# Kernel optimization log

Hardware: AMD Instinct MI355X
Metric: run time of the kernel (lower is better)

The kernel has to match this reference:

```python
import jax, jax.numpy as jnp
import numpy as np

B, H, W = 64, 16, 16
DIMS = [2048, 1024, 512, 256, 128, 1]


def _target_fc(x, w, b):
    # x: [B, in, H, W]; w: [B, out, in, 1, 1]; b: [B, out]
    # Equivalent to grouped 1x1 conv2d with groups=B (per-sample FC over channels).
    y = jnp.einsum('boi,bihw->bohw', w[:, :, :, 0, 0], x)
    return y + b[:, :, None, None]


def setup_inputs() -> dict:
    key = jax.random.key(0)
    ks = jax.random.split(key, 11)
    inp = {'x': jax.random.normal(ks[0], (B, DIMS[0], H, W), dtype=jnp.float32)}
    for i in range(5):
        din, dout = DIMS[i], DIMS[i + 1]
        scale = 1.0 / np.sqrt(din)
        inp[f'w{i+1}'] = jax.random.normal(ks[1 + 2 * i], (B, dout, din, 1, 1), dtype=jnp.float32) * scale
        inp[f'b{i+1}'] = jax.random.normal(ks[2 + 2 * i], (B, dout), dtype=jnp.float32) * scale
    return inp


def reference(x, w1, b1, w2, b2, w3, b3, w4, b4, w5, b5):
    q = jax.nn.sigmoid(_target_fc(x, w1, b1))
    q = jax.nn.sigmoid(_target_fc(q, w2, b2))
    q = jax.nn.sigmoid(_target_fc(q, w3, b3))
    q = jax.nn.sigmoid(_target_fc(q, w4, b4))
    q = _target_fc(q, w5, b5)
    return jnp.squeeze(q)  # [B, H, W]
```

## Files before the change

kernel.cpp:

```cpp
#include <hip/hip_runtime.h>
#include <hip/hip_bf16.h>
#include <cstdint>

#define DEVINL __device__ __forceinline__

typedef __attribute__((ext_vector_type(8))) short bf16x8;
typedef __attribute__((ext_vector_type(4))) float f32x4;

DEVINL unsigned short f2bf(float f) {
    union { float f; unsigned u; } v; v.f = f;
    unsigned r = v.u + 0x7fffu + ((v.u >> 16) & 1u);
    return (unsigned short)(r >> 16);
}
DEVINL float bf2f(unsigned short h) {
    union { unsigned u; float f; } v; v.u = ((unsigned)h) << 16;
    return v.f;
}

constexpr int BM = 64, BN = 256, BK = 32;
constexpr int PA  = 40;
constexpr int NSP = 256;

__global__ __launch_bounds__(256)
void xpose(const float* __restrict__ x, unsigned short* __restrict__ xT)
{
    __shared__ float sh[64][65];
    const int b   = blockIdx.y;
    const int kt  = blockIdx.x & 31;
    const int ntb = blockIdx.x >> 5;
    const int k0 = kt * 64, n0 = ntb * 64;

    const int r = threadIdx.x >> 4;
    const int c = (threadIdx.x & 15) * 4;

    const float* xb = x + ((size_t)b * 2048 + k0) * 256 + n0;
#pragma unroll
    for (int i = 0; i < 4; ++i) {
        float4 v = *(const float4*)(xb + (size_t)(r + 16 * i) * 256 + c);
        sh[r + 16 * i][c + 0] = v.x;
        sh[r + 16 * i][c + 1] = v.y;
        sh[r + 16 * i][c + 2] = v.z;
        sh[r + 16 * i][c + 3] = v.w;
    }
    __syncthreads();
#pragma unroll
    for (int i = 0; i < 4; ++i) {
        const int rr = r + 16 * i;
        ushort4 o;
        o.x = f2bf(sh[c + 0][rr]);
        o.y = f2bf(sh[c + 1][rr]);
        o.z = f2bf(sh[c + 2][rr]);
        o.w = f2bf(sh[c + 3][rr]);
        *(ushort4*)(xT + ((size_t)b * NSP + n0 + rr) * 2048 + k0 + c) = o;
    }
}

__global__ __launch_bounds__(256, 4)
void fc_gemm(const float* __restrict__ Wt, const float* __restrict__ bias,
             const unsigned short* __restrict__ X, unsigned short* __restrict__ Yt,
             int M, int K)
{
    const int b  = blockIdx.x;
    const int m0 = blockIdx.y * BM;

    __shared__ __align__(128) unsigned short pool[64 * PA + 2 * 256 * 32];
    unsigned short* sA = pool;
    unsigned short* sB = pool + 64 * PA;

    const int tid  = threadIdx.x;
    const int lane = tid & 63;
    const int wid  = tid >> 6;
    const int wn   = wid * 64;
    const int fr   = lane & 15;
    const int fo   = (lane >> 4) * 8;

    const int am = tid >> 2, ac = (tid & 3) * 8;
    const float* Wb = Wt + (size_t)b * M * K + (size_t)m0 * K + (size_t)am * K + ac;

    const int grow = wid * 64 + (lane >> 2);
    const int gchk = ((lane & 3) ^ ((lane >> 3) & 3)) * 8;
    const unsigned short* Xb = X + (size_t)b * NSP * K;

    const int bslot = ((lane >> 4) ^ ((fr >> 1) & 3)) * 8;

    const int NT = K / BK;

    float4 aS[2];

#define LOADA(k0) { aS[0] = *(const float4*)(Wb + (k0)); \
                    aS[1] = *(const float4*)(Wb + (k0) + 4); }
#define STOREA()  { ushort4 p0, p1; \
        p0.x = f2bf(aS[0].x); p0.y = f2bf(aS[0].y); p0.z = f2bf(aS[0].z); p0.w = f2bf(aS[0].w); \
        p1.x = f2bf(aS[1].x); p1.y = f2bf(aS[1].y); p1.z = f2bf(aS[1].z); p1.w = f2bf(aS[1].w); \
        *(ushort4*)&sA[am * PA + ac]     = p0; \
        *(ushort4*)&sA[am * PA + ac + 4] = p1; }
#define GLOADB(k0, bufofs) { \
    _Pragma("unroll") for (int i = 0; i < 4; ++i) { \
        const unsigned short* src_ = Xb + (size_t)(grow + i * 16) * K + (k0) + gchk; \
        const unsigned short* dst_ = sB + (bufofs) + (wid * 64 + i * 16) * 32; \
        __builtin_amdgcn_global_load_lds( \
            (const __attribute__((address_space(1))) void*)src_, \
            (__attribute__((address_space(3))) void*)dst_, 16, 0, 0); } }

    f32x4 acc[4][4] = {};

    LOADA(0)
    GLOADB(0, 0)
    STOREA()
    __syncthreads();

#pragma unroll 1
    for (int t = 0; t < NT; ++t) {
        const int pr = (t & 1) * (256 * 32);
        const int pw = ((t + 1) & 1) * (256 * 32);
        if (t + 1 < NT) { LOADA((t + 1) * BK) GLOADB((t + 1) * BK, pw) }

        bf16x8 af[4], bf[4];
#pragma unroll
        for (int i = 0; i < 4; ++i)
            af[i] = *(const bf16x8*)&sA[(i * 16 + fr) * PA + fo];
#pragma unroll
        for (int i = 0; i < 4; ++i)
            bf[i] = *(const bf16x8*)&sB[pr + (wn + i * 16 + fr) * 32 + bslot];

        asm volatile("s_waitcnt lgkmcnt(0)" ::: "memory");
        __builtin_amdgcn_s_barrier();

        if (t + 1 < NT) STOREA()

#pragma unroll
        for (int mi = 0; mi < 4; ++mi)
#pragma unroll
            for (int ni = 0; ni < 4; ++ni)
                acc[mi][ni] = __builtin_amdgcn_mfma_f32_16x16x32_bf16(af[mi], bf[ni], acc[mi][ni], 0, 0, 0);

        __syncthreads();
    }
#undef LOADA
#undef STOREA
#undef GLOADB

    const int hi4 = (lane >> 4) * 4;
#pragma unroll 1
    for (int ph = 0; ph < 2; ++ph) {
        if ((wn >> 7) == ph) {
#pragma unroll
            for (int mi = 0; mi < 4; ++mi) {
#pragma unroll
                for (int ni = 0; ni < 4; ++ni) {
                    const int r  = (wn & 127) + ni * 16 + fr;
                    const int mb = mi * 16 + hi4;
                    f32x4 v = acc[mi][ni];
                    ushort4 o;
#pragma unroll
                    for (int q = 0; q < 4; ++q) {
                        float yv = v[q] + bias[(size_t)b * M + m0 + mb + q];
                        yv = 1.0f / (1.0f + __expf(-yv));
                        ((unsigned short*)&o)[q] = f2bf(yv);
                    }
                    *(ushort4*)&pool[r * 72 + mb] = o;
                }
            }
        }
        __syncthreads();
        const int r = tid >> 3;
        const int c = (tid & 7) * 8;
#pragma unroll
        for (int it = 0; it < 4; ++it) {
            const int rr = r + it * 32;
            uint4 v = *(const uint4*)&pool[rr * 72 + c];
            *(uint4*)&Yt[((size_t)b * NSP + ph * 128 + rr) * M + m0 + c] = v;
        }
        __syncthreads();
    }
}

__global__ void fc_final(const unsigned short* __restrict__ A4,
                         const float* __restrict__ W5,
                         const float* __restrict__ B5,
                         float* __restrict__ out)
{
    const int b = blockIdx.x;
    const int t = threadIdx.x;
    const unsigned short* row = A4 + ((size_t)b * NSP + t) * 128;
    const float* w = W5 + (size_t)b * 128;
    float acc = B5[b];
#pragma unroll
    for (int k = 0; k < 128; k += 8) {
        uint4 v = *(const uint4*)(row + k);
        acc += bf2f((unsigned short)(v.x & 0xffff)) * w[k+0];
        acc += bf2f((unsigned short)(v.x >> 16))    * w[k+1];
        acc += bf2f((unsigned short)(v.y & 0xffff)) * w[k+2];
        acc += bf2f((unsigned short)(v.y >> 16))    * w[k+3];
        acc += bf2f((unsigned short)(v.z & 0xffff)) * w[k+4];
        acc += bf2f((unsigned short)(v.z >> 16))    * w[k+5];
        acc += bf2f((unsigned short)(v.w & 0xffff)) * w[k+6];
        acc += bf2f((unsigned short)(v.w >> 16))    * w[k+7];
    }
    out[b * NSP + t] = acc;
}

extern "C" void kernel_launch(void* const* d_in, const int* in_sizes, int n_in,
                              void* d_out, int out_size, void* d_ws, size_t ws_size,
                              hipStream_t stream)
{
    const float* x  = (const float*)d_in[0];
    const float* w1 = (const float*)d_in[1];
    const float* b1 = (const float*)d_in[2];
    const float* w2 = (const float*)d_in[3];
    const float* b2 = (const float*)d_in[4];
    const float* w3 = (const float*)d_in[5];
    const float* b3 = (const float*)d_in[6];
    const float* w4 = (const float*)d_in[7];
    const float* b4 = (const float*)d_in[8];
    const float* w5 = (const float*)d_in[9];
    const float* b5 = (const float*)d_in[10];

    unsigned short* ws0 = (unsigned short*)d_ws;

    const size_t XT = (size_t)64 * 256 * 2048;
    unsigned short* xT   = ws0;
    unsigned short* act1 = ws0 + XT;
    unsigned short* act2 = ws0;
    unsigned short* act3 = ws0 + (size_t)64 * 256 * 512;
    unsigned short* act4 = ws0 + (size_t)64 * 256 * (512 + 256);

    xpose<<<dim3(128, 64), dim3(256), 0, stream>>>(x, xT);
    fc_gemm<<<dim3(64, 16), dim3(256), 0, stream>>>(w1, b1, xT,   act1, 1024, 2048);
    fc_gemm<<<dim3(64,  8), dim3(256), 0, stream>>>(w2, b2, act1, act2,  512, 1024);
    fc_gemm<<<dim3(64,  4), dim3(256), 0, stream>>>(w3, b3, act2, act3,  256,  512);
    fc_gemm<<<dim3(64,  2), dim3(256), 0, stream>>>(w4, b4, act3, act4,  128,  256);
    fc_final<<<dim3(64), dim3(256), 0, stream>>>(act4, w5, b5, (float*)d_out);
}
```

Before: 372.8 us.

## Fuse transpose and all FC layers into one persistent kernel with per-sample barriers

Replaces six launches (transpose, four GEMMs, final dot) with a single kernel of 512 blocks, eight blocks per sample, synchronized by a per-sample global atomic barrier between layers. This removes launch gaps and lets later small layers follow immediately. In exchange, later layers leave most blocks idle (only 4 or 2 of 8 work), the barrier relies on all 512 blocks being co-resident, and layer 1 now runs in 512 blocks rather than 1024. A memset is added to reset the barrier counters.

```diff
diff --git a/kernel.cpp b/kernel.cpp
--- a/kernel.cpp
+++ b/kernel.cpp
@@ -21,53 +21,43 @@
 constexpr int PA  = 40;
 constexpr int NSP = 256;
 
-__global__ __launch_bounds__(256)
-void xpose(const float* __restrict__ x, unsigned short* __restrict__ xT)
-{
-    __shared__ float sh[64][65];
-    const int b   = blockIdx.y;
-    const int kt  = blockIdx.x & 31;
-    const int ntb = blockIdx.x >> 5;
-    const int k0 = kt * 64, n0 = ntb * 64;
-
-    const int r = threadIdx.x >> 4;
-    const int c = (threadIdx.x & 15) * 4;
-
-    const float* xb = x + ((size_t)b * 2048 + k0) * 256 + n0;
-#pragma unroll
-    for (int i = 0; i < 4; ++i) {
-        float4 v = *(const float4*)(xb + (size_t)(r + 16 * i) * 256 + c);
-        sh[r + 16 * i][c + 0] = v.x;
-        sh[r + 16 * i][c + 1] = v.y;
-        sh[r + 16 * i][c + 2] = v.z;
-        sh[r + 16 * i][c + 3] = v.w;
-    }
+constexpr size_t ARENA  = 1048576;
+constexpr size_t XT_OFF = 0;
+constexpr size_t A1_OFF = 524288;
+constexpr size_t A2_OFF = 786432;
+constexpr size_t A3_OFF = 917504;
+constexpr size_t A4_OFF = 983040;
+constexpr size_t BAR_BYTE_OFF = (size_t)64 * ARENA * 2;
+
+DEVINL void gbar(unsigned* cnt, unsigned* gen)
+{
     __syncthreads();
-#pragma unroll
-    for (int i = 0; i < 4; ++i) {
-        const int rr = r + 16 * i;
-        ushort4 o;
-        o.x = f2bf(sh[c + 0][rr]);
-        o.y = f2bf(sh[c + 1][rr]);
-        o.z = f2bf(sh[c + 2][rr]);
-        o.w = f2bf(sh[c + 3][rr]);
-        *(ushort4*)(xT + ((size_t)b * NSP + n0 + rr) * 2048 + k0 + c) = o;
-    }
-}
-
-__global__ __launch_bounds__(256, 4)
-void fc_gemm(const float* __restrict__ Wt, const float* __restrict__ bias,
-             const unsigned short* __restrict__ X, unsigned short* __restrict__ Yt,
-             int M, int K)
-{
-    const int b  = blockIdx.x;
-    const int m0 = blockIdx.y * BM;
-
-    __shared__ __align__(128) unsigned short pool[64 * PA + 2 * 256 * 32];
+    if (threadIdx.x == 0) {
+        unsigned g = __hip_atomic_load(gen, __ATOMIC_RELAXED, __HIP_MEMORY_SCOPE_AGENT);
+        __threadfence();
+        unsigned v = __hip_atomic_fetch_add(cnt, 1u, __ATOMIC_RELAXED, __HIP_MEMORY_SCOPE_AGENT);
+        if (v == 7u) {
+            __hip_atomic_store(cnt, 0u, __ATOMIC_RELAXED, __HIP_MEMORY_SCOPE_AGENT);
+            __hip_atomic_store(gen, g + 1u, __ATOMIC_RELEASE, __HIP_MEMORY_SCOPE_AGENT);
+        } else {
+            while (__hip_atomic_load(gen, __ATOMIC_ACQUIRE, __HIP_MEMORY_SCOPE_AGENT) == g)
+                __builtin_amdgcn_s_sleep(8);
+        }
+        __threadfence();
+    }
+    __syncthreads();
+}
+
+DEVINL void gemm_bn256(const float* __restrict__ Wfull,
+                       const float* __restrict__ biasb,
+                       const unsigned short* __restrict__ xb,
+                       unsigned short* __restrict__ yb,
+                       const int M, const int K, const int m0,
+                       unsigned short* pool, const int tid)
+{
     unsigned short* sA = pool;
     unsigned short* sB = pool + 64 * PA;
 
-    const int tid  = threadIdx.x;
     const int lane = tid & 63;
     const int wid  = tid >> 6;
     const int wn   = wid * 64;
@@ -75,12 +65,10 @@
     const int fo   = (lane >> 4) * 8;
 
     const int am = tid >> 2, ac = (tid & 3) * 8;
-    const float* Wb = Wt + (size_t)b * M * K + (size_t)m0 * K + (size_t)am * K + ac;
+    const float* Wb = Wfull + (size_t)(m0 + am) * K + ac;
 
     const int grow = wid * 64 + (lane >> 2);
     const int gchk = ((lane & 3) ^ ((lane >> 3) & 3)) * 8;
-    const unsigned short* Xb = X + (size_t)b * NSP * K;
-
     const int bslot = ((lane >> 4) ^ ((fr >> 1) & 3)) * 8;
 
     const int NT = K / BK;
@@ -96,7 +84,7 @@
         *(ushort4*)&sA[am * PA + ac + 4] = p1; }
 #define GLOADB(k0, bufofs) { \
     _Pragma("unroll") for (int i = 0; i < 4; ++i) { \
-        const unsigned short* src_ = Xb + (size_t)(grow + i * 16) * K + (k0) + gchk; \
+        const unsigned short* src_ = xb + (size_t)(grow + i * 16) * K + (k0) + gchk; \
         const unsigned short* dst_ = sB + (bufofs) + (wid * 64 + i * 16) * 32; \
         __builtin_amdgcn_global_load_lds( \
             (const __attribute__((address_space(1))) void*)src_, \
@@ -154,7 +142,7 @@
                     ushort4 o;
 #pragma unroll
                     for (int q = 0; q < 4; ++q) {
-                        float yv = v[q] + bias[(size_t)b * M + m0 + mb + q];
+                        float yv = v[q] + biasb[m0 + mb + q];
                         yv = 1.0f / (1.0f + __expf(-yv));
                         ((unsigned short*)&o)[q] = f2bf(yv);
                     }
@@ -169,35 +157,108 @@
         for (int it = 0; it < 4; ++it) {
             const int rr = r + it * 32;
             uint4 v = *(const uint4*)&pool[rr * 72 + c];
-            *(uint4*)&Yt[((size_t)b * NSP + ph * 128 + rr) * M + m0 + c] = v;
+            *(uint4*)&yb[(size_t)(ph * 128 + rr) * M + m0 + c] = v;
         }
         __syncthreads();
     }
 }
 
-__global__ void fc_final(const unsigned short* __restrict__ A4,
-                         const float* __restrict__ W5,
-                         const float* __restrict__ B5,
-                         float* __restrict__ out)
-{
-    const int b = blockIdx.x;
-    const int t = threadIdx.x;
-    const unsigned short* row = A4 + ((size_t)b * NSP + t) * 128;
-    const float* w = W5 + (size_t)b * 128;
-    float acc = B5[b];
-#pragma unroll
-    for (int k = 0; k < 128; k += 8) {
-        uint4 v = *(const uint4*)(row + k);
-        acc += bf2f((unsigned short)(v.x & 0xffff)) * w[k+0];
-        acc += bf2f((unsigned short)(v.x >> 16))    * w[k+1];
-        acc += bf2f((unsigned short)(v.y & 0xffff)) * w[k+2];
-        acc += bf2f((unsigned short)(v.y >> 16))    * w[k+3];
-        acc += bf2f((unsigned short)(v.z & 0xffff)) * w[k+4];
-        acc += bf2f((unsigned short)(v.z >> 16))    * w[k+5];
-        acc += bf2f((unsigned short)(v.w & 0xffff)) * w[k+6];
-        acc += bf2f((unsigned short)(v.w >> 16))    * w[k+7];
-    }
-    out[b * NSP + t] = acc;
+__global__ __launch_bounds__(256, 4)
+void fused_net(const float* __restrict__ x,
+               const float* __restrict__ w1, const float* __restrict__ b1,
+               const float* __restrict__ w2, const float* __restrict__ b2,
+               const float* __restrict__ w3, const float* __restrict__ b3,
+               const float* __restrict__ w4, const float* __restrict__ b4,
+               const float* __restrict__ w5, const float* __restrict__ b5,
+               float* __restrict__ out, unsigned short* __restrict__ act,
+               unsigned* __restrict__ bar)
+{
+    __shared__ __align__(128) unsigned char smem_raw[64 * PA * 2 + 2 * 256 * 32 * 2];
+    unsigned short* pool = (unsigned short*)smem_raw;
+
+    const int g = blockIdx.x;
+    const int b = g >> 3;
+    const int s = g & 7;
+    const int tid = threadIdx.x;
+
+    unsigned short* arena = act + (size_t)b * ARENA;
+    unsigned* cnt = bar + b * 64;
+    unsigned* gen = cnt + 1;
+
+    {
+        float (*sh)[65] = (float(*)[65])smem_raw;
+        const int r  = tid >> 4;
+        const int c4 = (tid & 15) * 4;
+#pragma unroll 1
+        for (int kt = 0; kt < 4; ++kt) {
+#pragma unroll 1
+            for (int nt = 0; nt < 4; ++nt) {
+                const int k0 = s * 256 + kt * 64, n0 = nt * 64;
+                const float* xb = x + ((size_t)b * 2048 + k0) * 256 + n0;
+#pragma unroll
+                for (int i = 0; i < 4; ++i) {
+                    float4 v = *(const float4*)(xb + (size_t)(r + 16 * i) * 256 + c4);
+                    sh[r + 16 * i][c4 + 0] = v.x;
+                    sh[r + 16 * i][c4 + 1] = v.y;
+                    sh[r + 16 * i][c4 + 2] = v.z;
+                    sh[r + 16 * i][c4 + 3] = v.w;
+                }
+                __syncthreads();
+#pragma unroll
+                for (int i = 0; i < 4; ++i) {
+                    const int rr = r + 16 * i;
+                    ushort4 o;
+                    o.x = f2bf(sh[c4 + 0][rr]);
+                    o.y = f2bf(sh[c4 + 1][rr]);
+                    o.z = f2bf(sh[c4 + 2][rr]);
+                    o.w = f2bf(sh[c4 + 3][rr]);
+                    *(ushort4*)(arena + XT_OFF + (size_t)(n0 + rr) * 2048 + k0 + c4) = o;
+                }
+                __syncthreads();
+            }
+        }
+    }
+    gbar(cnt, gen);
+
+    gemm_bn256(w1 + (size_t)b * 1024 * 2048, b1 + (size_t)b * 1024,
+               arena + XT_OFF, arena + A1_OFF, 1024, 2048, s * 64, pool, tid);
+    gemm_bn256(w1 + (size_t)b * 1024 * 2048, b1 + (size_t)b * 1024,
+               arena + XT_OFF, arena + A1_OFF, 1024, 2048, (s + 8) * 64, pool, tid);
+    gbar(cnt, gen);
+
+    gemm_bn256(w2 + (size_t)b * 512 * 1024, b2 + (size_t)b * 512,
+               arena + A1_OFF, arena + A2_OFF, 512, 1024, s * 64, pool, tid);
+    gbar(cnt, gen);
+
+    if (s < 4)
+        gemm_bn256(w3 + (size_t)b * 256 * 512, b3 + (size_t)b * 256,
+                   arena + A2_OFF, arena + A3_OFF, 256, 512, s * 64, pool, tid);
+    gbar(cnt, gen);
+
+    if (s < 2)
+        gemm_bn256(w4 + (size_t)b * 128 * 256, b4 + (size_t)b * 128,
+                   arena + A3_OFF, arena + A4_OFF, 128, 256, s * 64, pool, tid);
+    gbar(cnt, gen);
+
+    if (tid < 32) {
+        const int n = s * 32 + tid;
+        const unsigned short* row = arena + A4_OFF + (size_t)n * 128;
+        const float* w = w5 + (size_t)b * 128;
+        float accv = b5[b];
+#pragma unroll
+        for (int k = 0; k < 128; k += 8) {
+            uint4 v = *(const uint4*)(row + k);
+            accv += bf2f((unsigned short)(v.x & 0xffff)) * w[k+0];
+            accv += bf2f((unsigned short)(v.x >> 16))    * w[k+1];
+            accv += bf2f((unsigned short)(v.y & 0xffff)) * w[k+2];
+            accv += bf2f((unsigned short)(v.y >> 16))    * w[k+3];
+            accv += bf2f((unsigned short)(v.z & 0xffff)) * w[k+4];
+            accv += bf2f((unsigned short)(v.z >> 16))    * w[k+5];
+            accv += bf2f((unsigned short)(v.w & 0xffff)) * w[k+6];
+            accv += bf2f((unsigned short)(v.w >> 16))    * w[k+7];
+        }
+        out[b * NSP + n] = accv;
+    }
 }
 
 extern "C" void kernel_launch(void* const* d_in, const int* in_sizes, int n_in,
@@ -216,19 +277,12 @@
     const float* w5 = (const float*)d_in[9];
     const float* b5 = (const float*)d_in[10];
 
-    unsigned short* ws0 = (unsigned short*)d_ws;
-
-    const size_t XT = (size_t)64 * 256 * 2048;
-    unsigned short* xT   = ws0;
-    unsigned short* act1 = ws0 + XT;
-    unsigned short* act2 = ws0;
-    unsigned short* act3 = ws0 + (size_t)64 * 256 * 512;
-    unsigned short* act4 = ws0 + (size_t)64 * 256 * (512 + 256);
-
-    xpose<<<dim3(128, 64), dim3(256), 0, stream>>>(x, xT);
-    fc_gemm<<<dim3(64, 16), dim3(256), 0, stream>>>(w1, b1, xT,   act1, 1024, 2048);
-    fc_gemm<<<dim3(64,  8), dim3(256), 0, stream>>>(w2, b2, act1, act2,  512, 1024);
-    fc_gemm<<<dim3(64,  4), dim3(256), 0, stream>>>(w3, b3, act2, act3,  256,  512);
-    fc_gemm<<<dim3(64,  2), dim3(256), 0, stream>>>(w4, b4, act3, act4,  128,  256);
-    fc_final<<<dim3(64), dim3(256), 0, stream>>>(act4, w5, b5, (float*)d_out);
-}
+    unsigned short* act = (unsigned short*)d_ws;
+    unsigned* bar = (unsigned*)((char*)d_ws + BAR_BYTE_OFF);
+
+    hipMemsetAsync((void*)bar, 0, 64 * 256, stream);
+
+    fused_net<<<dim3(512), dim3(256), 0, stream>>>(
+        x, w1, b1, w2, b2, w3, b3, w4, b4, w5, b5,
+        (float*)d_out, act, bar);
+}
```

Result: slower. 817.8 us (+119.4%).

## Prefetch weight tiles two K-steps ahead with register double-buffering

Applied to the files above, without the earlier changes.

The weight (A) operand of the grouped FC GEMM is now loaded into two alternating register buffers, two K-steps ahead of use. The main loop is manually unrolled by two so the buffers can swap roles. The end-of-step __syncthreads is replaced by an explicit vmcnt(2) wait plus a barrier, so the outstanding A loads for step t+2 can remain in flight while the LDS-bound B loads for step t+1 are complete. This aims to hide global-load latency of the fp32 weights behind MFMA work, at the cost of more registers and a reliance on every layer's K/BK being even and on the hardware completing vector loads in issue order.

```diff
diff --git a/kernel.cpp b/kernel.cpp
--- a/kernel.cpp
+++ b/kernel.cpp
@@ -20,6 +20,7 @@
 constexpr int BM = 64, BN = 256, BK = 32;
 constexpr int PA  = 40;
 constexpr int NSP = 256;
+constexpr int BUF = 256 * 32;
 
 __global__ __launch_bounds__(256)
 void xpose(const float* __restrict__ x, unsigned short* __restrict__ xT)
@@ -63,7 +64,7 @@
     const int b  = blockIdx.x;
     const int m0 = blockIdx.y * BM;
 
-    __shared__ __align__(128) unsigned short pool[64 * PA + 2 * 256 * 32];
+    __shared__ __align__(128) unsigned short pool[64 * PA + 2 * BUF];
     unsigned short* sA = pool;
     unsigned short* sB = pool + 64 * PA;
 
@@ -85,13 +86,13 @@
 
     const int NT = K / BK;
 
-    float4 aS[2];
-
-#define LOADA(k0) { aS[0] = *(const float4*)(Wb + (k0)); \
-                    aS[1] = *(const float4*)(Wb + (k0) + 4); }
-#define STOREA()  { ushort4 p0, p1; \
-        p0.x = f2bf(aS[0].x); p0.y = f2bf(aS[0].y); p0.z = f2bf(aS[0].z); p0.w = f2bf(aS[0].w); \
-        p1.x = f2bf(aS[1].x); p1.y = f2bf(aS[1].y); p1.z = f2bf(aS[1].z); p1.w = f2bf(aS[1].w); \
+    float4 aSa[2], aSb[2];
+
+#define LOADA2(dst, k0) { dst[0] = *(const float4*)(Wb + (k0)); \
+                          dst[1] = *(const float4*)(Wb + (k0) + 4); }
+#define STOREA(src)  { ushort4 p0, p1; \
+        p0.x = f2bf(src[0].x); p0.y = f2bf(src[0].y); p0.z = f2bf(src[0].z); p0.w = f2bf(src[0].w); \
+        p1.x = f2bf(src[1].x); p1.y = f2bf(src[1].y); p1.z = f2bf(src[1].z); p1.w = f2bf(src[1].w); \
         *(ushort4*)&sA[am * PA + ac]     = p0; \
         *(ushort4*)&sA[am * PA + ac + 4] = p1; }
 #define GLOADB(k0, bufofs) { \
@@ -104,39 +105,43 @@
 
     f32x4 acc[4][4] = {};
 
-    LOADA(0)
     GLOADB(0, 0)
-    STOREA()
-    __syncthreads();
+    LOADA2(aSa, 0)
+    LOADA2(aSb, BK)
+    STOREA(aSa)
+    asm volatile("s_waitcnt lgkmcnt(0)" ::: "memory");
+    __builtin_amdgcn_s_barrier();
+
+#define KSTEP(t_, CONS, FILL) { \
+    const int tt = (t_); \
+    const int pr = (tt & 1) * BUF; \
+    const int pw = ((tt + 1) & 1) * BUF; \
+    if (tt + 1 < NT) GLOADB((tt + 1) * BK, pw) \
+    if (tt + 2 < NT) LOADA2(FILL, (tt + 2) * BK) \
+    bf16x8 af[4], bfv[4]; \
+    _Pragma("unroll") for (int i = 0; i < 4; ++i) \
+        af[i] = *(const bf16x8*)&sA[(i * 16 + fr) * PA + fo]; \
+    _Pragma("unroll") for (int i = 0; i < 4; ++i) \
+        bfv[i] = *(const bf16x8*)&sB[pr + (wn + i * 16 + fr) * 32 + bslot]; \
+    asm volatile("s_waitcnt lgkmcnt(0)" ::: "memory"); \
+    __builtin_amdgcn_s_barrier();                       \
+    if (tt + 1 < NT) STOREA(CONS)                       \
+    _Pragma("unroll") for (int mi = 0; mi < 4; ++mi) \
+        _Pragma("unroll") for (int ni = 0; ni < 4; ++ni) \
+            acc[mi][ni] = __builtin_amdgcn_mfma_f32_16x16x32_bf16(af[mi], bfv[ni], acc[mi][ni], 0, 0, 0); \
+    if (tt + 2 < NT) { asm volatile("s_waitcnt vmcnt(2)" ::: "memory"); } \
+    else             { asm volatile("s_waitcnt vmcnt(0)" ::: "memory"); } \
+    asm volatile("s_waitcnt lgkmcnt(0)" ::: "memory"); \
+    __builtin_amdgcn_s_barrier();                       \
+}
 
 #pragma unroll 1
-    for (int t = 0; t < NT; ++t) {
-        const int pr = (t & 1) * (256 * 32);
-        const int pw = ((t + 1) & 1) * (256 * 32);
-        if (t + 1 < NT) { LOADA((t + 1) * BK) GLOADB((t + 1) * BK, pw) }
-
-        bf16x8 af[4], bf[4];
-#pragma unroll
-        for (int i = 0; i < 4; ++i)
-            af[i] = *(const bf16x8*)&sA[(i * 16 + fr) * PA + fo];
-#pragma unroll
-        for (int i = 0; i < 4; ++i)
-            bf[i] = *(const bf16x8*)&sB[pr + (wn + i * 16 + fr) * 32 + bslot];
-
-        asm volatile("s_waitcnt lgkmcnt(0)" ::: "memory");
-        __builtin_amdgcn_s_barrier();
-
-        if (t + 1 < NT) STOREA()
-
-#pragma unroll
-        for (int mi = 0; mi < 4; ++mi)
-#pragma unroll
-            for (int ni = 0; ni < 4; ++ni)
-                acc[mi][ni] = __builtin_amdgcn_mfma_f32_16x16x32_bf16(af[mi], bf[ni], acc[mi][ni], 0, 0, 0);
-
-        __syncthreads();
-    }
-#undef LOADA
+    for (int t = 0; t < NT; t += 2) {
+        KSTEP(t,     aSb, aSa)
+        KSTEP(t + 1, aSa, aSb)
+    }
+#undef KSTEP
+#undef LOADA2
 #undef STOREA
 #undef GLOADB
 
```

Measured after the change: 653.8 us. 75.4% more time.
